# Kernel tuning notes

Hardware: AMD Instinct MI355X
Metric: run time of the kernel (lower is better)

## Reference

```python
import jax, jax.numpy as jnp
import numpy as np

DIM = 256
NUM_HEADS = 8
HEAD_DIM = DIM // NUM_HEADS  # 32 (MQA: k/v projected to a single head)
RPE_DIM = 128
P = 10            # cpb table resolution per axis ('bilinear_4_10')
MAX_VALUE = 4.0
LOG_SCALE = 512.0
LOG2_8 = 3.0      # np.log2(8)


def _trilinear_sample(table, grid):
    """torch F.grid_sample 3D, mode='bilinear', padding_mode='zeros', align_corners=True.
    table: [C, D, H, W]; grid: [M, 3] with (x,y,z) in [-1,1] -> returns [C, M]."""
    C, D, H, W = table.shape
    x = (grid[:, 0] + 1.0) * 0.5 * (W - 1)
    y = (grid[:, 1] + 1.0) * 0.5 * (H - 1)
    z = (grid[:, 2] + 1.0) * 0.5 * (D - 1)
    x0f, y0f, z0f = jnp.floor(x), jnp.floor(y), jnp.floor(z)
    wx1, wy1, wz1 = x - x0f, y - y0f, z - z0f
    wx0, wy0, wz0 = 1.0 - wx1, 1.0 - wy1, 1.0 - wz1
    x0 = x0f.astype(jnp.int32); x1 = x0 + 1
    y0 = y0f.astype(jnp.int32); y1 = y0 + 1
    z0 = z0f.astype(jnp.int32); z1 = z0 + 1

    def corner(iz, iy, ix, w):
        inb = (iz >= 0) & (iz < D) & (iy >= 0) & (iy < H) & (ix >= 0) & (ix < W)
        v = table[:, jnp.clip(iz, 0, D - 1), jnp.clip(iy, 0, H - 1), jnp.clip(ix, 0, W - 1)]
        return v * jnp.where(inb, w, 0.0)[None, :]

    return (corner(z0, y0, x0, wz0 * wy0 * wx0) + corner(z0, y0, x1, wz0 * wy0 * wx1)
          + corner(z0, y1, x0, wz0 * wy1 * wx0) + corner(z0, y1, x1, wz0 * wy1 * wx1)
          + corner(z1, y0, x0, wz1 * wy0 * wx0) + corner(z1, y0, x1, wz1 * wy0 * wx1)
          + corner(z1, y1, x0, wz1 * wy1 * wx0) + corner(z1, y1, x1, wz1 * wy1 * wx1))


def setup_inputs() -> dict:
    rng = jax.random.key(0)
    ks = jax.random.split(rng, 12)
    B, nQ, nK = 2, 256, 2048
    s = 0.02
    return {
        "query": jax.random.normal(ks[0], (nQ, B, DIM), jnp.float32),
        "key": jax.random.normal(ks[1], (nK, B, DIM), jnp.float32),
        "reference_point": jax.random.normal(ks[2], (B, nQ, 8, 3), jnp.float32),
        "reference_angle": jax.random.normal(ks[3], (B, nQ), jnp.float32),
        "xyz_vol": jax.random.normal(ks[4], (B, nK, 3), jnp.float32),
        "q_w": jax.random.normal(ks[5], (DIM, DIM), jnp.float32) * s,
        "q_b": jnp.zeros((DIM,), jnp.float32),
        "k_w": jax.random.normal(ks[6], (DIM, HEAD_DIM), jnp.float32) * s,
        "k_b": jnp.zeros((HEAD_DIM,), jnp.float32),
        "v_w": jax.random.normal(ks[7], (DIM, HEAD_DIM), jnp.float32) * s,
        "v_b": jnp.zeros((HEAD_DIM,), jnp.float32),
        "proj_w": jax.random.normal(ks[8], (DIM, DIM), jnp.float32) * s,
        "proj_b": jnp.zeros((DIM,), jnp.float32),
        "cpb_w1": jax.random.normal(ks[9], (8, 3, RPE_DIM), jnp.float32) * s,
        "cpb_b1": jnp.zeros((8, RPE_DIM), jnp.float32),
        "cpb_w2": jax.random.normal(ks[10], (8, RPE_DIM, NUM_HEADS), jnp.float32) * s,
    }


def reference(query, key, reference_point, reference_angle, xyz_vol,
              q_w, q_b, k_w, k_b, v_w, v_b, proj_w, proj_b,
              cpb_w1, cpb_b1, cpb_w2):
    B, nQ = reference_point.shape[:2]
    nK = xyz_vol.shape[1]
    q_in = jnp.transpose(query, (1, 0, 2))  # [B, nQ, DIM]
    k_in = jnp.transpose(key, (1, 0, 2))    # [B, nK, DIM]

    # CPB MLP evaluated on the fixed coords table -> per-corner tables [8, NUM_HEADS, P, P, P]
    lin = jnp.linspace(-MAX_VALUE, MAX_VALUE, P, dtype=jnp.float32)
    coords = jnp.stack(jnp.meshgrid(lin, lin, lin, indexing='ij'), axis=-1)  # [P,P,P,3]
    hid = jax.nn.relu(jnp.einsum('pqrc,icd->ipqrd', coords, cpb_w1) + cpb_b1[:, None, None, None, :])
    tables = jnp.einsum('ipqrd,idh->ihpqr', hid, cpb_w2)

    # log-scaled relative deltas for all 8 corners (angle_type=='' -> no rotation branch)
    d = reference_point[:, :, None, :, :] - xyz_vol[:, None, :, None, :]  # [B,nQ,nK,8,3]
    d = jnp.sign(d) * jnp.log2(jnp.abs(d) * LOG_SCALE + 1.0) / LOG2_8 / MAX_VALUE
    grids = jnp.moveaxis(d, 3, 0).reshape(8, -1, 3)  # [8, B*nQ*nK, 3]

    sampled = jax.vmap(_trilinear_sample)(tables, grids)  # [8, NUM_HEADS, M]
    rpe = jnp.transpose(sampled.sum(0).reshape(NUM_HEADS, B, nQ, nK), (1, 0, 2, 3))  # [B,H,nQ,nK]

    scale = HEAD_DIM ** -0.5
    q = (q_in @ q_w + q_b).reshape(B, nQ, NUM_HEADS, HEAD_DIM)
    k = k_in @ k_w + k_b  # [B, nK, HEAD_DIM] (single shared KV head)
    v = k_in @ v_w + v_b
    attn = jnp.einsum('bqhd,bkd->bhqk', q * scale, k) + rpe
    attn = jax.nn.softmax(attn, axis=-1)
    x = jnp.einsum('bhqk,bkd->bqhd', attn, v).reshape(B, nQ, DIM)
    x = x @ proj_w + proj_b
    return jnp.transpose(x, (1, 0, 2)), attn
```

## Files before the change

### kernel.cpp

```cpp
#include <hip/hip_runtime.h>
#include <hip/hip_bf16.h>
#include <cstdint>

#define NQ 256
#define NK 2048
#define BB 2
#define SCALE 0.17677669529663687f

#define TB_OFF 0u
#define QP_OFF 128000u
#define KT_OFF 652288u
#define VP_OFF 1176576u

typedef unsigned short u16;
typedef _Float16 h16;
union U16x8 { uint4 u; h16 h[8]; };

__global__ __launch_bounds__(512) void k_prep(const float* __restrict__ query,
                                              const float* __restrict__ key,
                                              const float* __restrict__ qw,
                                              const float* __restrict__ qb,
                                              const float* __restrict__ kw,
                                              const float* __restrict__ kb,
                                              const float* __restrict__ vw,
                                              const float* __restrict__ vb,
                                              const float* __restrict__ w1g,
                                              const float* __restrict__ b1g,
                                              const float* __restrict__ w2g,
                                              u16* __restrict__ tb,
                                              float* __restrict__ qp,
                                              float* __restrict__ kpT,
                                              float* __restrict__ vp) {
  __shared__ __align__(16) char smraw[16 * 257 * 4];
  int bid = blockIdx.x, t = threadIdx.x;

  if (bid < 256) {
    float (*rows)[257] = (float(*)[257])smraw;
    int b = bid >> 7, kc = bid & 127;
    for (int idx = t; idx < 4096; idx += 512) {
      int r = idx >> 8, m = idx & 255;
      rows[r][m] = key[((kc * 16 + r) * BB + b) * 256 + m];
    }
    __syncthreads();
    int ks = t >> 5, d = t & 31;
    float a = kb[d], av = vb[d];
    #pragma unroll 4
    for (int m = 0; m < 256; ++m) {
      float rv = rows[ks][m];
      a  = fmaf(rv, kw[m * 32 + d], a);
      av = fmaf(rv, vw[m * 32 + d], av);
    }
    int k = kc * 16 + ks;
    vp[(b * NK + k) * 32 + d] = av;
    __syncthreads();
    float* f1 = (float*)smraw;
    f1[d * 16 + ks] = a;
    __syncthreads();
    int dd = t >> 4, kk = t & 15;
    kpT[(b * 32 + dd) * NK + kc * 16 + kk] = f1[dd * 16 + kk];
  } else if (bid < 320) {
    float (*rows)[257] = (float(*)[257])smraw;
    int qg = bid - 256;
    for (int idx = t; idx < 2048; idx += 512) {
      int r = idx >> 8, m = idx & 255;
      int g = qg * 8 + r, b = g >> 8, q = g & 255;
      rows[r][m] = query[(q * BB + b) * 256 + m];
    }
    __syncthreads();
    int r = t >> 6, c0 = (t & 63) * 4;
    int g = qg * 8 + r;
    float4 acc = *(const float4*)&qb[c0];
    #pragma unroll 4
    for (int m = 0; m < 256; ++m) {
      float rv = rows[r][m];
      float4 w4 = *(const float4*)&qw[m * 256 + c0];
      acc.x = fmaf(rv, w4.x, acc.x); acc.y = fmaf(rv, w4.y, acc.y);
      acc.z = fmaf(rv, w4.z, acc.z); acc.w = fmaf(rv, w4.w, acc.w);
    }
    float4 o; o.x = acc.x * SCALE; o.y = acc.y * SCALE; o.z = acc.z * SCALE; o.w = acc.w * SCALE;
    *(float4*)&qp[g * 256 + c0] = o;
  } else {
    float* w1 = (float*)smraw;
    float* b1 = w1 + 384;
    float* w2 = b1 + 128;
    int ib = bid - 320;
    int i = ib >> 2, cc = ib & 3;
    for (int idx = t; idx < 384; idx += 512) w1[idx] = w1g[i * 384 + idx];
    if (t < 128) b1[t] = b1g[i * 128 + t];
    for (int idx = t; idx < 1024; idx += 512) w2[idx] = w2g[i * 1024 + idx];
    __syncthreads();
    if (t < 250) {
      int cell = cc * 250 + t;
      int z = cell / 100, y = (cell / 10) % 10, x = cell % 10;
      const float step = 8.0f / 9.0f;
      float cz = -4.f + z * step, cy = -4.f + y * step, cx = -4.f + x * step;
      float o0 = 0, o1 = 0, o2 = 0, o3 = 0, o4 = 0, o5 = 0, o6 = 0, o7 = 0;
      for (int d = 0; d < 128; ++d) {
        float h = fmaxf(fmaf(cz, w1[d], fmaf(cy, w1[128 + d], fmaf(cx, w1[256 + d], b1[d]))), 0.f);
        const float* w2r = &w2[d * 8];
        o0 = fmaf(h, w2r[0], o0); o1 = fmaf(h, w2r[1], o1);
        o2 = fmaf(h, w2r[2], o2); o3 = fmaf(h, w2r[3], o3);
        o4 = fmaf(h, w2r[4], o4); o5 = fmaf(h, w2r[5], o5);
        o6 = fmaf(h, w2r[6], o6); o7 = fmaf(h, w2r[7], o7);
      }
      U16x8 R;
      R.h[0] = (h16)o0; R.h[1] = (h16)o1; R.h[2] = (h16)o2; R.h[3] = (h16)o3;
      R.h[4] = (h16)o4; R.h[5] = (h16)o5; R.h[6] = (h16)o6; R.h[7] = (h16)o7;
      *(uint4*)&tb[i * 8000 + cell * 8] = R.u;
    }
  }
}

struct Axis { int o0, o1; float w0, w1; };

static __device__ __forceinline__ Axis axis_setup(float dv, int stride) {
  float g = copysignf(__log2f(fmaf(fabsf(dv), 512.f, 1.f)) * (1.f / 12.f), dv);
  float p = fmaf(g, 4.5f, 4.5f);
  float f = floorf(p);
  int i0 = (int)f;
  float w1v = p - f;
  float w0v = 1.f - w1v;
  Axis a;
  a.w0 = ((unsigned)i0 <= 9u) ? w0v : 0.f;
  a.w1 = ((unsigned)(i0 + 1) <= 9u) ? w1v : 0.f;
  int c0 = min(max(i0, 0), 9);
  int c1 = min(max(i0 + 1, 0), 9);
  a.o0 = c0 * stride;
  a.o1 = c1 * stride;
  return a;
}

#define DO_CORNER(CU, W, J) do { float ww = (W); \
  acc[0][J] = fmaf((float)(CU).h[0], ww, acc[0][J]); \
  acc[1][J] = fmaf((float)(CU).h[1], ww, acc[1][J]); \
  acc[2][J] = fmaf((float)(CU).h[2], ww, acc[2][J]); \
  acc[3][J] = fmaf((float)(CU).h[3], ww, acc[3][J]); \
  acc[4][J] = fmaf((float)(CU).h[4], ww, acc[4][J]); \
  acc[5][J] = fmaf((float)(CU).h[5], ww, acc[5][J]); \
  acc[6][J] = fmaf((float)(CU).h[6], ww, acc[6][J]); \
  acc[7][J] = fmaf((float)(CU).h[7], ww, acc[7][J]); } while (0)

__global__ __launch_bounds__(1024, 4) void k_mega(const u16* __restrict__ tbw,
                                                  const float* __restrict__ qp,
                                                  const float* __restrict__ kpT,
                                                  const float* __restrict__ xyz,
                                                  const float* __restrict__ refp,
                                                  const float* __restrict__ vp,
                                                  const float* __restrict__ pw,
                                                  const float* __restrict__ pb,
                                                  float* __restrict__ attn,
                                                  float* __restrict__ out) {
  __shared__ __align__(16) char un[131072];
  __shared__ __align__(16) float red4[2][8][8][32];
  __shared__ __align__(16) float qrow[2][256];
  __shared__ __align__(16) float rp[2][24];
  __shared__ __align__(16) float red[2][64];
  u16* tb = (u16*)un;
  float* p = (float*)un;

  int t = threadIdx.x;
  int b = blockIdx.x >> 7, qc = blockIdx.x & 127;
  for (int idx = t; idx < 8000; idx += 1024)
    ((uint4*)tb)[idx] = ((const uint4*)tbw)[idx];
  if (t < 128) {
    int qh2 = t >> 6, c = t & 63;
    ((float4*)qrow[qh2])[c] = ((const float4*)(qp + (b * 256 + qc * 2 + qh2) * 256))[c];
  } else if (t < 140) {
    int idx = t - 128;
    int qh2 = idx / 6, c = idx % 6;
    ((float4*)rp[qh2])[c] = ((const float4*)(refp + (b * 256 + qc * 2 + qh2) * 24))[c];
  }
  __syncthreads();

  int wv = t >> 6, l = t & 63;
  int qh = wv >> 3, wvl = wv & 7;
  int k0 = wvl * 256 + l * 4;
  float acc[8][4] = {};

  const float* kT = kpT + b * (32 * NK);
  #pragma unroll 2
  for (int dq = 0; dq < 8; ++dq) {
    const float* kp0 = kT + (dq * 4) * NK + k0;
    float4 kv0 = *(const float4*)(kp0);
    float4 kv1 = *(const float4*)(kp0 + NK);
    float4 kv2 = *(const float4*)(kp0 + 2 * NK);
    float4 kv3 = *(const float4*)(kp0 + 3 * NK);
    #pragma unroll
    for (int h = 0; h < 8; ++h) {
      float4 qv = *(const float4*)&qrow[qh][h * 32 + dq * 4];
      acc[h][0] = fmaf(qv.x, kv0.x, fmaf(qv.y, kv1.x, fmaf(qv.z, kv2.x, fmaf(qv.w, kv3.x, acc[h][0]))));
      acc[h][1] = fmaf(qv.x, kv0.y, fmaf(qv.y, kv1.y, fmaf(qv.z, kv2.y, fmaf(qv.w, kv3.y, acc[h][1]))));
      acc[h][2] = fmaf(qv.x, kv0.z, fmaf(qv.y, kv1.z, fmaf(qv.z, kv2.z, fmaf(qv.w, kv3.z, acc[h][2]))));
      acc[h][3] = fmaf(qv.x, kv0.w, fmaf(qv.y, kv1.w, fmaf(qv.z, kv2.w, fmaf(qv.w, kv3.w, acc[h][3]))));
    }
  }

  {
    const float* xp = xyz + (size_t)(b * NK + k0) * 3;
    float4 X0 = *(const float4*)(xp);
    float4 X1 = *(const float4*)(xp + 4);
    float4 X2 = *(const float4*)(xp + 8);
    float xv[4] = { X0.x, X0.w, X1.z, X2.y };
    float yv[4] = { X0.y, X1.x, X1.w, X2.z };
    float zv[4] = { X0.z, X1.y, X2.x, X2.w };
    #pragma unroll 1
    for (int i = 0; i < 8; ++i) {
      float rx = rp[qh][i * 3 + 0];
      float ry = rp[qh][i * 3 + 1];
      float rz = rp[qh][i * 3 + 2];
      const u16* tp = tb + i * 8000;
      #pragma unroll
      for (int j = 0; j < 4; ++j) {
        Axis ax = axis_setup(rx - xv[j], 8);
        Axis ay = axis_setup(ry - yv[j], 80);
        Axis az = axis_setup(rz - zv[j], 800);
        float w00 = az.w0 * ay.w0, w01 = az.w0 * ay.w1;
        float w10 = az.w1 * ay.w0, w11 = az.w1 * ay.w1;
        U16x8 u;
        u.u = *(const uint4*)(tp + az.o0 + ay.o0 + ax.o0); DO_CORNER(u, w00 * ax.w0, j);
        u.u = *(const uint4*)(tp + az.o0 + ay.o0 + ax.o1); DO_CORNER(u, w00 * ax.w1, j);
        u.u = *(const uint4*)(tp + az.o0 + ay.o1 + ax.o0); DO_CORNER(u, w01 * ax.w0, j);
        u.u = *(const uint4*)(tp + az.o0 + ay.o1 + ax.o1); DO_CORNER(u, w01 * ax.w1, j);
        u.u = *(const uint4*)(tp + az.o1 + ay.o0 + ax.o0); DO_CORNER(u, w10 * ax.w0, j);
        u.u = *(const uint4*)(tp + az.o1 + ay.o0 + ax.o1); DO_CORNER(u, w10 * ax.w1, j);
        u.u = *(const uint4*)(tp + az.o1 + ay.o1 + ax.o0); DO_CORNER(u, w11 * ax.w0, j);
        u.u = *(const uint4*)(tp + az.o1 + ay.o1 + ax.o1); DO_CORNER(u, w11 * ax.w1, j);
      }
    }
  }

  float mx[8];
  #pragma unroll
  for (int h = 0; h < 8; ++h) {
    float m = fmaxf(fmaxf(acc[h][0], acc[h][1]), fmaxf(acc[h][2], acc[h][3]));
    #pragma unroll
    for (int off = 32; off >= 1; off >>= 1) m = fmaxf(m, __shfl_xor(m, off, 64));
    mx[h] = m;
  }
  if (l == 0) {
    #pragma unroll
    for (int h = 0; h < 8; ++h) red[qh][h * 8 + wvl] = mx[h];
  }
  __syncthreads();
  #pragma unroll
  for (int h = 0; h < 8; ++h) {
    float4 r0 = *(const float4*)&red[qh][h * 8];
    float4 r1 = *(const float4*)&red[qh][h * 8 + 4];
    mx[h] = fmaxf(fmaxf(fmaxf(r0.x, r0.y), fmaxf(r0.z, r0.w)),
                  fmaxf(fmaxf(r1.x, r1.y), fmaxf(r1.z, r1.w)));
  }
  __syncthreads();
  float sm[8];
  #pragma unroll
  for (int h = 0; h < 8; ++h) {
    acc[h][0] = __expf(acc[h][0] - mx[h]);
    acc[h][1] = __expf(acc[h][1] - mx[h]);
    acc[h][2] = __expf(acc[h][2] - mx[h]);
    acc[h][3] = __expf(acc[h][3] - mx[h]);
    float s = (acc[h][0] + acc[h][1]) + (acc[h][2] + acc[h][3]);
    #pragma unroll
    for (int off = 32; off >= 1; off >>= 1) s += __shfl_xor(s, off, 64);
    sm[h] = s;
  }
  if (l == 0) {
    #pragma unroll
    for (int h = 0; h < 8; ++h) red[qh][h * 8 + wvl] = sm[h];
  }
  __syncthreads();
  #pragma unroll
  for (int h = 0; h < 8; ++h) {
    float4 r0 = *(const float4*)&red[qh][h * 8];
    float4 r1 = *(const float4*)&red[qh][h * 8 + 4];
    float s = ((r0.x + r0.y) + (r0.z + r0.w)) + ((r1.x + r1.y) + (r1.z + r1.w));
    float inv = 1.f / s;
    float4 pv;
    pv.x = acc[h][0] * inv; pv.y = acc[h][1] * inv;
    pv.z = acc[h][2] * inv; pv.w = acc[h][3] * inv;
    *(float4*)&p[(qh * 8 + h) * 2048 + k0] = pv;
  }
  __syncthreads();

  #pragma unroll
  for (int c = 0; c < 8; ++c) {
    int flat = (c * 1024 + t) * 4;
    int qh2 = flat >> 14, h2 = (flat >> 11) & 7, kk = flat & 2047;
    float4 pv4 = *(const float4*)&p[(qh2 * 8 + h2) * 2048 + kk];
    *(float4*)&attn[((size_t)((b * 8 + h2) * 256 + (qc * 2 + qh2))) * 2048 + kk] = pv4;
  }

  {
    int ch = wv >> 1, pqh = wv & 1;
    int ks2 = l >> 3, dq = l & 7;
    float a2[8][4] = {};
    const float* vbase = vp + ((size_t)(b * NK + ch * 256)) * 32 + dq * 4;
    const float* prow = p + pqh * 16384 + ch * 256;
    #pragma unroll 2
    for (int kk = 0; kk < 32; ++kk) {
      int ko = kk * 8 + ks2;
      float4 v4 = *(const float4*)&vbase[ko * 32];
      #pragma unroll
      for (int h = 0; h < 8; ++h) {
        float pvv = prow[h * 2048 + ko];
        a2[h][0] = fmaf(pvv, v4.x, a2[h][0]);
        a2[h][1] = fmaf(pvv, v4.y, a2[h][1]);
        a2[h][2] = fmaf(pvv, v4.z, a2[h][2]);
        a2[h][3] = fmaf(pvv, v4.w, a2[h][3]);
      }
    }
    #pragma unroll
    for (int off = 8; off <= 32; off <<= 1) {
      #pragma unroll
      for (int h = 0; h < 8; ++h) {
        a2[h][0] += __shfl_xor(a2[h][0], off, 64);
        a2[h][1] += __shfl_xor(a2[h][1], off, 64);
        a2[h][2] += __shfl_xor(a2[h][2], off, 64);
        a2[h][3] += __shfl_xor(a2[h][3], off, 64);
      }
    }
    if (ks2 == 0) {
      #pragma unroll
      for (int h = 0; h < 8; ++h) {
        float4 w4; w4.x = a2[h][0]; w4.y = a2[h][1]; w4.z = a2[h][2]; w4.w = a2[h][3];
        *(float4*)&red4[pqh][ch][h][dq * 4] = w4;
      }
    }
  }
  __syncthreads();
  if (t < 512) {
    int pqh = t >> 8, m = t & 255;
    int h = m >> 5, d = m & 31;
    float s = 0.f;
    #pragma unroll
    for (int ch = 0; ch < 8; ++ch) s += red4[pqh][ch][h][d];
    qrow[pqh][m] = s;
  }
  __syncthreads();

  {
    float* scratch = (float*)red4;
    int c = t & 255, half = (t >> 8) & 1, pqh = t >> 9;
    int m0 = half * 128;
    float a = 0.f;
    #pragma unroll 4
    for (int m = 0; m < 128; ++m) {
      a = fmaf(qrow[pqh][m0 + m], pw[(m0 + m) * 256 + c], a);
    }
    scratch[(pqh * 2 + half) * 256 + c] = a;
  }
  __syncthreads();
  if (t < 512) {
    float* scratch = (float*)red4;
    int pqh = t >> 8, c = t & 255;
    float v = scratch[(pqh * 2) * 256 + c] + scratch[(pqh * 2 + 1) * 256 + c] + pb[c];
    int q = qc * 2 + pqh;
    out[(q * BB + b) * 256 + c] = v;
  }
}

extern "C" void kernel_launch(void* const* d_in, const int* in_sizes, int n_in,
                              void* d_out, int out_size, void* d_ws, size_t ws_size,
                              hipStream_t stream) {
  const float* query = (const float*)d_in[0];
  const float* key   = (const float*)d_in[1];
  const float* refp  = (const float*)d_in[2];
  const float* xyz   = (const float*)d_in[4];
  const float* qw    = (const float*)d_in[5];
  const float* qb    = (const float*)d_in[6];
  const float* kw    = (const float*)d_in[7];
  const float* kb    = (const float*)d_in[8];
  const float* vw    = (const float*)d_in[9];
  const float* vb    = (const float*)d_in[10];
  const float* pw    = (const float*)d_in[11];
  const float* pb    = (const float*)d_in[12];
  const float* w1    = (const float*)d_in[13];
  const float* b1    = (const float*)d_in[14];
  const float* w2    = (const float*)d_in[15];

  char* ws = (char*)d_ws;
  u16*   tb  = (u16*)(ws + TB_OFF);
  float* qp  = (float*)(ws + QP_OFF);
  float* kpT = (float*)(ws + KT_OFF);
  float* vp  = (float*)(ws + VP_OFF);
  float* out  = (float*)d_out;
  float* attn = out + 131072;

  hipLaunchKernelGGL(k_prep, dim3(352), dim3(512),  0, stream,
                     query, key, qw, qb, kw, kb, vw, vb, w1, b1, w2, tb, qp, kpT, vp);
  hipLaunchKernelGGL(k_mega, dim3(256), dim3(1024), 0, stream,
                     tb, qp, kpT, xyz, refp, vp, pw, pb, attn, out);
}
```

Baseline: 193.6 us.

## Fuse prep and main kernels into one cooperative kernel with grid sync

Merges the projection/table-prep kernel into the main attention kernel, launched cooperatively with a grid-wide barrier in place of a second kernel launch. Prep work is re-split across 200 of the 256 blocks, with larger per-block tiles and k/v weights staged in shared memory. The attn tile is now written straight from registers instead of being staged through shared memory and written by a separate loop. Costs: the grid sync, a cooperative launch that requires all blocks to be co-resident, and fewer blocks doing prep work.

```diff
diff --git a/kernel.cpp b/kernel.cpp
--- a/kernel.cpp
+++ b/kernel.cpp
@@ -1,6 +1,9 @@
 #include <hip/hip_runtime.h>
+#include <hip/hip_cooperative_groups.h>
 #include <hip/hip_bf16.h>
 #include <cstdint>
+
+namespace cg = cooperative_groups;
 
 #define NQ 256
 #define NK 2048
@@ -15,101 +18,6 @@
 typedef unsigned short u16;
 typedef _Float16 h16;
 union U16x8 { uint4 u; h16 h[8]; };
-
-__global__ __launch_bounds__(512) void k_prep(const float* __restrict__ query,
-                                              const float* __restrict__ key,
-                                              const float* __restrict__ qw,
-                                              const float* __restrict__ qb,
-                                              const float* __restrict__ kw,
-                                              const float* __restrict__ kb,
-                                              const float* __restrict__ vw,
-                                              const float* __restrict__ vb,
-                                              const float* __restrict__ w1g,
-                                              const float* __restrict__ b1g,
-                                              const float* __restrict__ w2g,
-                                              u16* __restrict__ tb,
-                                              float* __restrict__ qp,
-                                              float* __restrict__ kpT,
-                                              float* __restrict__ vp) {
-  __shared__ __align__(16) char smraw[16 * 257 * 4];
-  int bid = blockIdx.x, t = threadIdx.x;
-
-  if (bid < 256) {
-    float (*rows)[257] = (float(*)[257])smraw;
-    int b = bid >> 7, kc = bid & 127;
-    for (int idx = t; idx < 4096; idx += 512) {
-      int r = idx >> 8, m = idx & 255;
-      rows[r][m] = key[((kc * 16 + r) * BB + b) * 256 + m];
-    }
-    __syncthreads();
-    int ks = t >> 5, d = t & 31;
-    float a = kb[d], av = vb[d];
-    #pragma unroll 4
-    for (int m = 0; m < 256; ++m) {
-      float rv = rows[ks][m];
-      a  = fmaf(rv, kw[m * 32 + d], a);
-      av = fmaf(rv, vw[m * 32 + d], av);
-    }
-    int k = kc * 16 + ks;
-    vp[(b * NK + k) * 32 + d] = av;
-    __syncthreads();
-    float* f1 = (float*)smraw;
-    f1[d * 16 + ks] = a;
-    __syncthreads();
-    int dd = t >> 4, kk = t & 15;
-    kpT[(b * 32 + dd) * NK + kc * 16 + kk] = f1[dd * 16 + kk];
-  } else if (bid < 320) {
-    float (*rows)[257] = (float(*)[257])smraw;
-    int qg = bid - 256;
-    for (int idx = t; idx < 2048; idx += 512) {
-      int r = idx >> 8, m = idx & 255;
-      int g = qg * 8 + r, b = g >> 8, q = g & 255;
-      rows[r][m] = query[(q * BB + b) * 256 + m];
-    }
-    __syncthreads();
-    int r = t >> 6, c0 = (t & 63) * 4;
-    int g = qg * 8 + r;
-    float4 acc = *(const float4*)&qb[c0];
-    #pragma unroll 4
-    for (int m = 0; m < 256; ++m) {
-      float rv = rows[r][m];
-      float4 w4 = *(const float4*)&qw[m * 256 + c0];
-      acc.x = fmaf(rv, w4.x, acc.x); acc.y = fmaf(rv, w4.y, acc.y);
-      acc.z = fmaf(rv, w4.z, acc.z); acc.w = fmaf(rv, w4.w, acc.w);
-    }
-    float4 o; o.x = acc.x * SCALE; o.y = acc.y * SCALE; o.z = acc.z * SCALE; o.w = acc.w * SCALE;
-    *(float4*)&qp[g * 256 + c0] = o;
-  } else {
-    float* w1 = (float*)smraw;
-    float* b1 = w1 + 384;
-    float* w2 = b1 + 128;
-    int ib = bid - 320;
-    int i = ib >> 2, cc = ib & 3;
-    for (int idx = t; idx < 384; idx += 512) w1[idx] = w1g[i * 384 + idx];
-    if (t < 128) b1[t] = b1g[i * 128 + t];
-    for (int idx = t; idx < 1024; idx += 512) w2[idx] = w2g[i * 1024 + idx];
-    __syncthreads();
-    if (t < 250) {
-      int cell = cc * 250 + t;
-      int z = cell / 100, y = (cell / 10) % 10, x = cell % 10;
-      const float step = 8.0f / 9.0f;
-      float cz = -4.f + z * step, cy = -4.f + y * step, cx = -4.f + x * step;
-      float o0 = 0, o1 = 0, o2 = 0, o3 = 0, o4 = 0, o5 = 0, o6 = 0, o7 = 0;
-      for (int d = 0; d < 128; ++d) {
-        float h = fmaxf(fmaf(cz, w1[d], fmaf(cy, w1[128 + d], fmaf(cx, w1[256 + d], b1[d]))), 0.f);
-        const float* w2r = &w2[d * 8];
-        o0 = fmaf(h, w2r[0], o0); o1 = fmaf(h, w2r[1], o1);
-        o2 = fmaf(h, w2r[2], o2); o3 = fmaf(h, w2r[3], o3);
-        o4 = fmaf(h, w2r[4], o4); o5 = fmaf(h, w2r[5], o5);
-        o6 = fmaf(h, w2r[6], o6); o7 = fmaf(h, w2r[7], o7);
-      }
-      U16x8 R;
-      R.h[0] = (h16)o0; R.h[1] = (h16)o1; R.h[2] = (h16)o2; R.h[3] = (h16)o3;
-      R.h[4] = (h16)o4; R.h[5] = (h16)o5; R.h[6] = (h16)o6; R.h[7] = (h16)o7;
-      *(uint4*)&tb[i * 8000 + cell * 8] = R.u;
-    }
-  }
-}
 
 struct Axis { int o0, o1; float w0, w1; };
 
@@ -140,26 +48,113 @@
   acc[6][J] = fmaf((float)(CU).h[6], ww, acc[6][J]); \
   acc[7][J] = fmaf((float)(CU).h[7], ww, acc[7][J]); } while (0)
 
-__global__ __launch_bounds__(1024, 4) void k_mega(const u16* __restrict__ tbw,
-                                                  const float* __restrict__ qp,
-                                                  const float* __restrict__ kpT,
-                                                  const float* __restrict__ xyz,
-                                                  const float* __restrict__ refp,
-                                                  const float* __restrict__ vp,
-                                                  const float* __restrict__ pw,
-                                                  const float* __restrict__ pb,
-                                                  float* __restrict__ attn,
-                                                  float* __restrict__ out) {
+__global__ __launch_bounds__(1024, 4) void k_all(
+    const float* __restrict__ query, const float* __restrict__ key,
+    const float* __restrict__ qw,    const float* __restrict__ qb,
+    const float* __restrict__ kw,    const float* __restrict__ kb,
+    const float* __restrict__ vw,    const float* __restrict__ vb,
+    const float* __restrict__ w1g,   const float* __restrict__ b1g,
+    const float* __restrict__ w2g,
+    const float* __restrict__ xyz,   const float* __restrict__ refp,
+    const float* __restrict__ pw,    const float* __restrict__ pb,
+    u16* __restrict__ tbw,   float* __restrict__ qp,
+    float* __restrict__ kpT, float* __restrict__ vp,
+    float* __restrict__ attn, float* __restrict__ out) {
   __shared__ __align__(16) char un[131072];
   __shared__ __align__(16) float red4[2][8][8][32];
   __shared__ __align__(16) float qrow[2][256];
   __shared__ __align__(16) float rp[2][24];
   __shared__ __align__(16) float red[2][64];
+
+  int bid = blockIdx.x, t = threadIdx.x;
+
+  if (bid < 128) {
+    float* rows = (float*)un;
+    float* kwl  = rows + 8192;
+    float* vwl  = kwl + 8192;
+    int b = bid >> 6, k0b = (bid & 63) * 32;
+    for (int i = t; i < 2048; i += 1024) {
+      int rr = i >> 6, c4 = i & 63;
+      ((float4*)rows)[i] = ((const float4*)key)[((k0b + rr) * 2 + b) * 64 + c4];
+    }
+    for (int i = t; i < 2048; i += 1024) ((float4*)kwl)[i] = ((const float4*)kw)[i];
+    for (int i = t; i < 2048; i += 1024) ((float4*)vwl)[i] = ((const float4*)vw)[i];
+    __syncthreads();
+    int ks = t >> 5, d = t & 31;
+    float a = kb[d], av = vb[d];
+    const float* rw = rows + ks * 256;
+    #pragma unroll 4
+    for (int m = 0; m < 256; ++m) {
+      float rv = rw[m];
+      a  = fmaf(rv, kwl[m * 32 + d], a);
+      av = fmaf(rv, vwl[m * 32 + d], av);
+    }
+    int k = k0b + ks;
+    vp[(b * NK + k) * 32 + d] = av;
+    __syncthreads();
+    float* f1 = (float*)un;
+    f1[d * 33 + ks] = a;
+    __syncthreads();
+    int dd = t >> 5, kk = t & 31;
+    kpT[(b * 32 + dd) * NK + k0b + kk] = f1[dd * 33 + kk];
+  } else if (bid < 192) {
+    float* rows = (float*)un;
+    int qg = bid - 128;
+    for (int i = t; i < 512; i += 1024) {
+      int rr = i >> 6, c4 = i & 63;
+      int g = qg * 8 + rr, bq = g >> 8, q = g & 255;
+      ((float4*)rows)[i] = ((const float4*)query)[(q * BB + bq) * 64 + c4];
+    }
+    __syncthreads();
+    int r = t >> 7, c0 = (t & 127) * 2;
+    int g = qg * 8 + r;
+    const float* rw = rows + r * 256;
+    float2 acc2 = *(const float2*)&qb[c0];
+    #pragma unroll 4
+    for (int m = 0; m < 256; ++m) {
+      float rv = rw[m];
+      float2 w2v = *(const float2*)&qw[m * 256 + c0];
+      acc2.x = fmaf(rv, w2v.x, acc2.x);
+      acc2.y = fmaf(rv, w2v.y, acc2.y);
+    }
+    float2 o; o.x = acc2.x * SCALE; o.y = acc2.y * SCALE;
+    *(float2*)&qp[g * 256 + c0] = o;
+  } else if (bid < 200) {
+    float* w1 = (float*)un;
+    float* b1 = w1 + 384;
+    float* w2 = b1 + 128;
+    int i = bid - 192;
+    if (t < 384) w1[t] = w1g[i * 384 + t];
+    else if (t < 512) b1[t - 384] = b1g[i * 128 + (t - 384)];
+    if (t < 1024) w2[t] = w2g[i * 1024 + t];
+    __syncthreads();
+    if (t < 1000) {
+      int cell = t;
+      int z = cell / 100, y = (cell / 10) % 10, x = cell % 10;
+      const float step = 8.0f / 9.0f;
+      float cz = -4.f + z * step, cy = -4.f + y * step, cx = -4.f + x * step;
+      float o0 = 0, o1 = 0, o2 = 0, o3 = 0, o4 = 0, o5 = 0, o6 = 0, o7 = 0;
+      for (int d = 0; d < 128; ++d) {
+        float h = fmaxf(fmaf(cz, w1[d], fmaf(cy, w1[128 + d], fmaf(cx, w1[256 + d], b1[d]))), 0.f);
+        const float* w2r = &w2[d * 8];
+        o0 = fmaf(h, w2r[0], o0); o1 = fmaf(h, w2r[1], o1);
+        o2 = fmaf(h, w2r[2], o2); o3 = fmaf(h, w2r[3], o3);
+        o4 = fmaf(h, w2r[4], o4); o5 = fmaf(h, w2r[5], o5);
+        o6 = fmaf(h, w2r[6], o6); o7 = fmaf(h, w2r[7], o7);
+      }
+      U16x8 R;
+      R.h[0] = (h16)o0; R.h[1] = (h16)o1; R.h[2] = (h16)o2; R.h[3] = (h16)o3;
+      R.h[4] = (h16)o4; R.h[5] = (h16)o5; R.h[6] = (h16)o6; R.h[7] = (h16)o7;
+      *(uint4*)&tbw[i * 8000 + cell * 8] = R.u;
+    }
+  }
+
+  cg::this_grid().sync();
+
   u16* tb = (u16*)un;
   float* p = (float*)un;
-
-  int t = threadIdx.x;
-  int b = blockIdx.x >> 7, qc = blockIdx.x & 127;
+  int b = bid >> 7, qc = bid & 127;
+
   for (int idx = t; idx < 8000; idx += 1024)
     ((uint4*)tb)[idx] = ((const uint4*)tbw)[idx];
   if (t < 128) {
@@ -174,6 +169,7 @@
 
   int wv = t >> 6, l = t & 63;
   int qh = wv >> 3, wvl = wv & 7;
+  int q = qc * 2 + qh;
   int k0 = wvl * 256 + l * 4;
   float acc[8][4] = {};
 
@@ -277,16 +273,9 @@
     pv.x = acc[h][0] * inv; pv.y = acc[h][1] * inv;
     pv.z = acc[h][2] * inv; pv.w = acc[h][3] * inv;
     *(float4*)&p[(qh * 8 + h) * 2048 + k0] = pv;
-  }
-  __syncthreads();
-
-  #pragma unroll
-  for (int c = 0; c < 8; ++c) {
-    int flat = (c * 1024 + t) * 4;
-    int qh2 = flat >> 14, h2 = (flat >> 11) & 7, kk = flat & 2047;
-    float4 pv4 = *(const float4*)&p[(qh2 * 8 + h2) * 2048 + kk];
-    *(float4*)&attn[((size_t)((b * 8 + h2) * 256 + (qc * 2 + qh2))) * 2048 + kk] = pv4;
-  }
+    *(float4*)&attn[((size_t)((b * 8 + h) * 256 + q)) * 2048 + k0] = pv;
+  }
+  __syncthreads();
 
   {
     int ch = wv >> 1, pqh = wv & 1;
@@ -352,8 +341,8 @@
     float* scratch = (float*)red4;
     int pqh = t >> 8, c = t & 255;
     float v = scratch[(pqh * 2) * 256 + c] + scratch[(pqh * 2 + 1) * 256 + c] + pb[c];
-    int q = qc * 2 + pqh;
-    out[(q * BB + b) * 256 + c] = v;
+    int qq = qc * 2 + pqh;
+    out[(qq * BB + b) * 256 + c] = v;
   }
 }
 
@@ -384,8 +373,11 @@
   float* out  = (float*)d_out;
   float* attn = out + 131072;
 
-  hipLaunchKernelGGL(k_prep, dim3(352), dim3(512),  0, stream,
-                     query, key, qw, qb, kw, kb, vw, vb, w1, b1, w2, tb, qp, kpT, vp);
-  hipLaunchKernelGGL(k_mega, dim3(256), dim3(1024), 0, stream,
-                     tb, qp, kpT, xyz, refp, vp, pw, pb, attn, out);
+  void* args[] = { (void*)&query, (void*)&key, (void*)&qw, (void*)&qb,
+                   (void*)&kw, (void*)&kb, (void*)&vw, (void*)&vb,
+                   (void*)&w1, (void*)&b1, (void*)&w2,
+                   (void*)&xyz, (void*)&refp, (void*)&pw, (void*)&pb,
+                   (void*)&tb, (void*)&qp, (void*)&kpT, (void*)&vp,
+                   (void*)&attn, (void*)&out };
+  hipLaunchCooperativeKernel((void*)k_all, dim3(256), dim3(1024), args, 0, stream);
 }
```

New measurement: 244.4 us. +26.2%, slower.
